# Kernel optimization log

Hardware: AMD Instinct MI355X
Metric: run time of the kernel (lower is better)

## Reference

```python
import jax, jax.numpy as jnp
import numpy as np


def setup_inputs() -> dict:
    key = jax.random.key(0)
    ks = jax.random.split(key, 5)
    B, T, D, H = 32, 2048, 512, 512
    return {
        "x": jax.random.normal(ks[0], (B, T, D), dtype=jnp.float32),
        "W_w": jax.random.normal(ks[1], (4 * H, D), dtype=jnp.float32) * 0.05,
        "W_b": jax.random.normal(ks[2], (4 * H,), dtype=jnp.float32) * 0.05,
        "U_w": jax.random.normal(ks[3], (4 * H, H), dtype=jnp.float32) * 0.05,
        "U_b": jax.random.normal(ks[4], (4 * H,), dtype=jnp.float32) * 0.05,
        "alpha": jnp.ones((H,), dtype=jnp.float32),
    }


def reference(x, W_w, W_b, U_w, U_b, alpha):
    B, T, D = x.shape
    H = alpha.shape[0]
    # Precompute input projection for all timesteps: [B, T, 4H]
    wx = jnp.einsum("btd,gd->btg", x, W_w) + W_b
    h0 = jnp.zeros((B, H), dtype=x.dtype)
    c0 = jnp.zeros((B, H), dtype=x.dtype)

    def step(carry, wx_t):
        h, c = carry
        gates = wx_t + h @ U_w.T + U_b  # [B, 4H]
        i, f, o, g = jnp.split(gates, 4, axis=-1)
        i = jax.nn.sigmoid(i)
        f = jax.nn.sigmoid(f)
        o = jax.nn.sigmoid(o)
        g = jnp.tanh(g)
        c = alpha * (f * c + i * g)
        h = o * jnp.tanh(c)
        return (h, c), h

    (h, c), outs = jax.lax.scan(step, (h0, c0), jnp.swapaxes(wx, 0, 1))
    outs = jnp.swapaxes(outs, 0, 1)  # [B, T, H]
    return outs, (h, c)
```

## Files before the change

kernel.cpp:

```cpp
#include <hip/hip_runtime.h>

#define TT 2048
#define BB 32
#define HH 512
#define NWG 32

typedef _Float16 half8 __attribute__((ext_vector_type(8)));
typedef float f32x4 __attribute__((ext_vector_type(4)));

__device__ __forceinline__ float fsig(float x) { return 1.f / (1.f + __expf(-x)); }
__device__ __forceinline__ float ftanh_(float x) {
  x = fminf(fmaxf(x, -15.f), 15.f);
  float e = __expf(2.f * x);
  return (e - 1.f) / (e + 1.f);
}

__global__ void cvt_f32_f16(const float* __restrict__ in, _Float16* __restrict__ out, int n4) {
  int i = blockIdx.x * 256 + threadIdx.x;
  if (i >= n4) return;
  float4 v = ((const float4*)in)[i];
  union { _Float16 h[4]; unsigned long long u; } r;
  r.h[0] = (_Float16)v.x; r.h[1] = (_Float16)v.y;
  r.h[2] = (_Float16)v.z; r.h[3] = (_Float16)v.w;
  ((unsigned long long*)out)[i] = r.u;
}

__global__ __launch_bounds__(256, 2) void gemm_wx(const _Float16* __restrict__ A,
                                                  const _Float16* __restrict__ Bw,
                                                  _Float16* __restrict__ C) {
  const int bn = blockIdx.x;
  const int bm = blockIdx.y;
  const int tid = threadIdx.x;
  const int lane = tid & 63;
  const int w = tid >> 6;
  __shared__ _Float16 As[128 * 40];
  __shared__ _Float16 Bs[128 * 40];
  const int moff = (w & 1) * 64;
  const int noff = (w >> 1) * 64;
  const int fm = lane & 15;
  const int kq = lane >> 4;
  f32x4 acc[4][4] = {};
  for (int kt = 0; kt < 16; ++kt) {
#pragma unroll
    for (int e = 0; e < 2; ++e) {
      int ci = tid * 2 + e;
      int r = ci >> 2, c16 = ci & 3;
      half8 av = *(const half8*)(A + (size_t)(bm * 128 + r) * 512 + kt * 32 + c16 * 8);
      half8 bv = *(const half8*)(Bw + (size_t)(bn * 128 + r) * 512 + kt * 32 + c16 * 8);
      *(half8*)(As + r * 40 + c16 * 8) = av;
      *(half8*)(Bs + r * 40 + c16 * 8) = bv;
    }
    __syncthreads();
    half8 af[4], bf[4];
#pragma unroll
    for (int i = 0; i < 4; ++i) {
      af[i] = *(const half8*)(As + (moff + i * 16 + fm) * 40 + kq * 8);
      bf[i] = *(const half8*)(Bs + (noff + i * 16 + fm) * 40 + kq * 8);
    }
#pragma unroll
    for (int i = 0; i < 4; ++i)
#pragma unroll
      for (int j = 0; j < 4; ++j)
        acc[i][j] = __builtin_amdgcn_mfma_f32_16x16x32_f16(af[i], bf[j], acc[i][j], 0, 0, 0);
    __syncthreads();
  }
#pragma unroll
  for (int i = 0; i < 4; ++i) {
    int row = bm * 128 + moff + i * 16 + (lane >> 4) * 4;
#pragma unroll
    for (int j = 0; j < 4; ++j) {
      int col = bn * 128 + noff + j * 16 + (lane & 15);
#pragma unroll
      for (int r = 0; r < 4; ++r)
        C[(size_t)(row + r) * 2048 + col] = (_Float16)acc[i][j][r];
    }
  }
}

__global__ __launch_bounds__(256, 1) void slstm_scan(
    const _Float16* __restrict__ wx,
    const _Float16* __restrict__ U16,
    const float* __restrict__ Wb, const float* __restrict__ Ub,
    const float* __restrict__ alpha,
    _Float16* __restrict__ hex,
    float* __restrict__ out) {
  const int g = blockIdx.x;
  const int tid = threadIdx.x;
  const int lane = tid & 63;
  const int w = tid >> 6;
  const int mi = w & 1;
  const int qA = (w >> 1) * 2;
  const int ncol = lane & 15;
  const int kq = lane >> 4;
  const int am = mi * 16 + ncol;

  half8 Bf0[16], Bf1[16];
#pragma unroll
  for (int ks = 0; ks < 16; ++ks) {
    Bf0[ks] = *(const half8*)(U16 + (size_t)(qA * 512 + g * 16 + ncol) * 512 + ks * 32 + kq * 8);
    Bf1[ks] = *(const half8*)(U16 + (size_t)((qA + 1) * 512 + g * 16 + ncol) * 512 + ks * 32 + kq * 8);
  }

  const int eb = tid >> 3;
  const int jp = tid & 7;
  const int gj0 = g * 16 + jp * 2;
  float bias0[4], bias1[4];
#pragma unroll
  for (int q = 0; q < 4; ++q) {
    bias0[q] = Wb[q * 512 + gj0] + Ub[q * 512 + gj0];
    bias1[q] = Wb[q * 512 + gj0 + 1] + Ub[q * 512 + gj0 + 1];
  }
  const float al0 = alpha[gj0], al1 = alpha[gj0 + 1];
  float c0 = 0.f, c1 = 0.f;

  __shared__ float Sg[4 * 32 * 18];
  __shared__ _Float16 Swx[4 * 32 * 16];

  const int lq = tid >> 6;
  const int lb = (tid >> 1) & 31;
  const int lc = tid & 1;
  const _Float16* wxp = wx + (size_t)lb * TT * 2048 + lq * 512 + g * 16 + lc * 8;

  int spin_budget = 1 << 22;

  for (int t = 0; t < TT; ++t) {
    half8 wxv = *(const half8*)(wxp + (size_t)t * 2048);
    f32x4 acc0 = {0.f, 0.f, 0.f, 0.f}, acc1 = {0.f, 0.f, 0.f, 0.f};
    if (t > 0) {
      const unsigned long long* hb64 =
          (const unsigned long long*)(hex + (size_t)(t - 1) * (BB * HH) + (size_t)am * HH);
      union { unsigned long long u[2]; half8 h; } af[16];
      for (;;) {
        unsigned mx = 0;
#pragma unroll
        for (int ks = 0; ks < 16; ++ks) {
          af[ks].u[0] = __hip_atomic_load(hb64 + ks * 8 + kq * 2,
                                          __ATOMIC_RELAXED, __HIP_MEMORY_SCOPE_AGENT);
          af[ks].u[1] = __hip_atomic_load(hb64 + ks * 8 + kq * 2 + 1,
                                          __ATOMIC_RELAXED, __HIP_MEMORY_SCOPE_AGENT);
        }
#pragma unroll
        for (int ks = 0; ks < 16; ++ks) {
          unsigned a = (unsigned)af[ks].u[0], b = (unsigned)(af[ks].u[0] >> 32);
          unsigned c = (unsigned)af[ks].u[1], d = (unsigned)(af[ks].u[1] >> 32);
          mx = mx > a ? mx : a; mx = mx > b ? mx : b;
          mx = mx > c ? mx : c; mx = mx > d ? mx : d;
        }
        if (__all(mx < 0xFFFF0000u)) break;
        if (--spin_budget <= 0) break;
      }
#pragma unroll
      for (int ks = 0; ks < 16; ++ks) {
        acc0 = __builtin_amdgcn_mfma_f32_16x16x32_f16(af[ks].h, Bf0[ks], acc0, 0, 0, 0);
        acc1 = __builtin_amdgcn_mfma_f32_16x16x32_f16(af[ks].h, Bf1[ks], acc1, 0, 0, 0);
      }
    }
    *(half8*)(Swx + (lq * 32 + lb) * 16 + lc * 8) = wxv;
#pragma unroll
    for (int i = 0; i < 4; ++i) {
      int m = mi * 16 + kq * 4 + i;
      Sg[(qA * 32 + m) * 18 + ncol] = acc0[i];
      Sg[((qA + 1) * 32 + m) * 18 + ncol] = acc1[i];
    }
    __syncthreads();
    float p0[4], p1[4];
#pragma unroll
    for (int q = 0; q < 4; ++q) {
      const int so = (q * 32 + eb) * 18 + jp * 2;
      const int wo = (q * 32 + eb) * 16 + jp * 2;
      p0[q] = Sg[so] + (float)Swx[wo] + bias0[q];
      p1[q] = Sg[so + 1] + (float)Swx[wo + 1] + bias1[q];
    }
    float i0 = fsig(p0[0]), f0 = fsig(p0[1]), o0 = fsig(p0[2]), g0 = ftanh_(p0[3]);
    float i1 = fsig(p1[0]), f1 = fsig(p1[1]), o1 = fsig(p1[2]), g1 = ftanh_(p1[3]);
    c0 = al0 * (f0 * c0 + i0 * g0);
    c1 = al1 * (f1 * c1 + i1 * g1);
    float h0 = o0 * ftanh_(c0);
    float h1 = o1 * ftanh_(c1);
    union { _Float16 h[2]; unsigned int u; } pk;
    pk.h[0] = (_Float16)h0; pk.h[1] = (_Float16)h1;
    unsigned int* hx = (unsigned int*)hex + ((size_t)t * (BB * HH) + eb * HH + gj0) / 2;
    __hip_atomic_store(hx, pk.u, __ATOMIC_RELAXED, __HIP_MEMORY_SCOPE_AGENT);
    size_t ob = ((size_t)eb * TT + t) * HH + gj0;
    union { float f[2]; double d; } od;
    od.f[0] = h0; od.f[1] = h1;
    __builtin_nontemporal_store(od.d, (double*)(out + ob));
    if (t == TT - 1) {
      const size_t HB = (size_t)BB * TT * HH;
      out[HB + eb * HH + gj0] = h0;
      out[HB + eb * HH + gj0 + 1] = h1;
      out[HB + BB * HH + eb * HH + gj0] = c0;
      out[HB + BB * HH + eb * HH + gj0 + 1] = c1;
    }
    __syncthreads();
  }
}

extern "C" void kernel_launch(void* const* d_in, const int* in_sizes, int n_in,
                              void* d_out, int out_size, void* d_ws, size_t ws_size,
                              hipStream_t stream) {
  (void)in_sizes; (void)n_in; (void)out_size; (void)ws_size;
  const float* x  = (const float*)d_in[0];
  const float* Ww = (const float*)d_in[1];
  const float* Wb = (const float*)d_in[2];
  const float* Uw = (const float*)d_in[3];
  const float* Ub = (const float*)d_in[4];
  const float* al = (const float*)d_in[5];
  float* out = (float*)d_out;

  char* p = (char*)d_ws;
  _Float16* x16  = (_Float16*)p; p += (size_t)BB * TT * 512 * 2;
  _Float16* wx16 = (_Float16*)p; p += (size_t)BB * TT * 2048 * 2;
  _Float16* U16  = (_Float16*)p; p += (size_t)2048 * 512 * 2;
  _Float16* W16  = (_Float16*)p; p += (size_t)2048 * 512 * 2;
  _Float16* hexb = x16;

  cvt_f32_f16<<<32768, 256, 0, stream>>>(x, x16, BB * TT * 512 / 4);
  cvt_f32_f16<<<1024, 256, 0, stream>>>(Ww, W16, 2048 * 512 / 4);
  cvt_f32_f16<<<1024, 256, 0, stream>>>(Uw, U16, 2048 * 512 / 4);
  gemm_wx<<<dim3(16, 512), 256, 0, stream>>>(x16, W16, wx16);
  (void)hipMemsetAsync(hexb, 0xFF, (size_t)TT * BB * HH * 2, stream);
  slstm_scan<<<NWG, 256, 0, stream>>>(wx16, U16, Wb, Ub, al, hexb, out);
}
```

Measured before the change: 14.73 ms.

## Use tagged double-buffered h exchange and drop trailing per-step barrier

Replaces the full-history fp16 h exchange buffer (sentinel-filled with 0xFF) with a two-slot ring of 64-bit words, each holding a timestep tag in the high half and two fp16 h values in the low half. Readers spin until every tag matches t-1 instead of checking for the sentinel. The shared gate staging buffers are double-buffered by step parity, so the second __syncthreads per step is removed. This also shrinks the large memset to a tiny one. The risk is that slot reuse depends on the tag check and the spin budget, so a slow workgroup could be overwritten two steps ahead. That should be safe, because each step needs all workgroups' previous h.

```diff
diff --git a/kernel.cpp b/kernel.cpp
--- a/kernel.cpp
+++ b/kernel.cpp
@@ -82,7 +82,7 @@
     const _Float16* __restrict__ U16,
     const float* __restrict__ Wb, const float* __restrict__ Ub,
     const float* __restrict__ alpha,
-    _Float16* __restrict__ hex,
+    unsigned long long* __restrict__ hexq,
     float* __restrict__ out) {
   const int g = blockIdx.x;
   const int tid = threadIdx.x;
@@ -113,54 +113,50 @@
   const float al0 = alpha[gj0], al1 = alpha[gj0 + 1];
   float c0 = 0.f, c1 = 0.f;
 
-  __shared__ float Sg[4 * 32 * 18];
-  __shared__ _Float16 Swx[4 * 32 * 16];
+  __shared__ float Sg[2][4 * 32 * 18];
+  __shared__ _Float16 Swx[2][4 * 32 * 16];
 
   const int lq = tid >> 6;
   const int lb = (tid >> 1) & 31;
   const int lc = tid & 1;
   const _Float16* wxp = wx + (size_t)lb * TT * 2048 + lq * 512 + g * 16 + lc * 8;
 
-  int spin_budget = 1 << 22;
+  int budget = 1 << 22;
 
   for (int t = 0; t < TT; ++t) {
+    const int par = t & 1;
     half8 wxv = *(const half8*)(wxp + (size_t)t * 2048);
     f32x4 acc0 = {0.f, 0.f, 0.f, 0.f}, acc1 = {0.f, 0.f, 0.f, 0.f};
     if (t > 0) {
-      const unsigned long long* hb64 =
-          (const unsigned long long*)(hex + (size_t)(t - 1) * (BB * HH) + (size_t)am * HH);
-      union { unsigned long long u[2]; half8 h; } af[16];
-      for (;;) {
-        unsigned mx = 0;
+      const unsigned exp_tag = (unsigned)(t - 1);
+      const unsigned long long* hb = hexq + (size_t)((t - 1) & 1) * 8192 + (size_t)am * 256;
+      union { unsigned u[4]; half8 h; } af[16];
+      unsigned bad;
+      do {
+        bad = 0;
 #pragma unroll
         for (int ks = 0; ks < 16; ++ks) {
-          af[ks].u[0] = __hip_atomic_load(hb64 + ks * 8 + kq * 2,
-                                          __ATOMIC_RELAXED, __HIP_MEMORY_SCOPE_AGENT);
-          af[ks].u[1] = __hip_atomic_load(hb64 + ks * 8 + kq * 2 + 1,
-                                          __ATOMIC_RELAXED, __HIP_MEMORY_SCOPE_AGENT);
+#pragma unroll
+          for (int p = 0; p < 4; ++p) {
+            unsigned long long wv = __hip_atomic_load(
+                hb + ks * 16 + kq * 4 + p, __ATOMIC_RELAXED, __HIP_MEMORY_SCOPE_AGENT);
+            bad |= ((unsigned)(wv >> 32)) ^ exp_tag;
+            af[ks].u[p] = (unsigned)wv;
+          }
         }
-#pragma unroll
-        for (int ks = 0; ks < 16; ++ks) {
-          unsigned a = (unsigned)af[ks].u[0], b = (unsigned)(af[ks].u[0] >> 32);
-          unsigned c = (unsigned)af[ks].u[1], d = (unsigned)(af[ks].u[1] >> 32);
-          mx = mx > a ? mx : a; mx = mx > b ? mx : b;
-          mx = mx > c ? mx : c; mx = mx > d ? mx : d;
-        }
-        if (__all(mx < 0xFFFF0000u)) break;
-        if (--spin_budget <= 0) break;
-      }
+      } while (__any(bad != 0) && --budget > 0);
 #pragma unroll
       for (int ks = 0; ks < 16; ++ks) {
         acc0 = __builtin_amdgcn_mfma_f32_16x16x32_f16(af[ks].h, Bf0[ks], acc0, 0, 0, 0);
         acc1 = __builtin_amdgcn_mfma_f32_16x16x32_f16(af[ks].h, Bf1[ks], acc1, 0, 0, 0);
       }
     }
-    *(half8*)(Swx + (lq * 32 + lb) * 16 + lc * 8) = wxv;
+    *(half8*)(Swx[par] + (lq * 32 + lb) * 16 + lc * 8) = wxv;
 #pragma unroll
     for (int i = 0; i < 4; ++i) {
       int m = mi * 16 + kq * 4 + i;
-      Sg[(qA * 32 + m) * 18 + ncol] = acc0[i];
-      Sg[((qA + 1) * 32 + m) * 18 + ncol] = acc1[i];
+      Sg[par][(qA * 32 + m) * 18 + ncol] = acc0[i];
+      Sg[par][((qA + 1) * 32 + m) * 18 + ncol] = acc1[i];
     }
     __syncthreads();
     float p0[4], p1[4];
@@ -168,8 +164,8 @@
     for (int q = 0; q < 4; ++q) {
       const int so = (q * 32 + eb) * 18 + jp * 2;
       const int wo = (q * 32 + eb) * 16 + jp * 2;
-      p0[q] = Sg[so] + (float)Swx[wo] + bias0[q];
-      p1[q] = Sg[so + 1] + (float)Swx[wo + 1] + bias1[q];
+      p0[q] = Sg[par][so] + (float)Swx[par][wo] + bias0[q];
+      p1[q] = Sg[par][so + 1] + (float)Swx[par][wo + 1] + bias1[q];
     }
     float i0 = fsig(p0[0]), f0 = fsig(p0[1]), o0 = fsig(p0[2]), g0 = ftanh_(p0[3]);
     float i1 = fsig(p1[0]), f1 = fsig(p1[1]), o1 = fsig(p1[2]), g1 = ftanh_(p1[3]);
@@ -177,10 +173,11 @@
     c1 = al1 * (f1 * c1 + i1 * g1);
     float h0 = o0 * ftanh_(c0);
     float h1 = o1 * ftanh_(c1);
-    union { _Float16 h[2]; unsigned int u; } pk;
-    pk.h[0] = (_Float16)h0; pk.h[1] = (_Float16)h1;
-    unsigned int* hx = (unsigned int*)hex + ((size_t)t * (BB * HH) + eb * HH + gj0) / 2;
-    __hip_atomic_store(hx, pk.u, __ATOMIC_RELAXED, __HIP_MEMORY_SCOPE_AGENT);
+    union { _Float16 hh[2]; unsigned u; } pk;
+    pk.hh[0] = (_Float16)h0; pk.hh[1] = (_Float16)h1;
+    unsigned long long word = ((unsigned long long)(unsigned)t << 32) | (unsigned long long)pk.u;
+    __hip_atomic_store(hexq + (size_t)par * 8192 + (size_t)eb * 256 + g * 8 + jp, word,
+                       __ATOMIC_RELAXED, __HIP_MEMORY_SCOPE_AGENT);
     size_t ob = ((size_t)eb * TT + t) * HH + gj0;
     union { float f[2]; double d; } od;
     od.f[0] = h0; od.f[1] = h1;
@@ -192,7 +189,6 @@
       out[HB + BB * HH + eb * HH + gj0] = c0;
       out[HB + BB * HH + eb * HH + gj0 + 1] = c1;
     }
-    __syncthreads();
   }
 }
 
@@ -213,12 +209,13 @@
   _Float16* wx16 = (_Float16*)p; p += (size_t)BB * TT * 2048 * 2;
   _Float16* U16  = (_Float16*)p; p += (size_t)2048 * 512 * 2;
   _Float16* W16  = (_Float16*)p; p += (size_t)2048 * 512 * 2;
-  _Float16* hexb = x16;
+  unsigned long long* hexq = (unsigned long long*)p;
+  p += (size_t)2 * 32 * 256 * 8;
 
   cvt_f32_f16<<<32768, 256, 0, stream>>>(x, x16, BB * TT * 512 / 4);
   cvt_f32_f16<<<1024, 256, 0, stream>>>(Ww, W16, 2048 * 512 / 4);
   cvt_f32_f16<<<1024, 256, 0, stream>>>(Uw, U16, 2048 * 512 / 4);
   gemm_wx<<<dim3(16, 512), 256, 0, stream>>>(x16, W16, wx16);
-  (void)hipMemsetAsync(hexb, 0xFF, (size_t)TT * BB * HH * 2, stream);
-  slstm_scan<<<NWG, 256, 0, stream>>>(wx16, U16, Wb, Ub, al, hexb, out);
-}
+  (void)hipMemsetAsync(hexq, 0xFF, (size_t)2 * 32 * 256 * 8, stream);
+  slstm_scan<<<NWG, 256, 0, stream>>>(wx16, U16, Wb, Ub, al, hexq, out);
+}
```

After: 22.79 ms. +54.7%, slower.
